# Kernel optimization log

Hardware: AMD Instinct MI355X
Metric: run time of the kernel (lower is better)

Reference implementation:

```python
import jax, jax.numpy as jnp
from jax import lax
import numpy as np

N, C, H, W = 8, 128, 96, 96
G, K = 8, 3                      # groups, kernel_size
GC = C // G                      # group channels = 16
STRIDE, PAD, DIL = 1, 1, 1
OFFSET_SCALE = 1.0
OM_DIM = int(np.ceil(G * K * K * 3 / 8) * 8)   # 216 (== G*K*K*3, no padding)
GN_EPS = 1e-5


def setup_inputs() -> dict:
    key = jax.random.key(0)
    ks = jax.random.split(key, 7)
    inp = {
        "input": jax.random.normal(ks[0], (N, C, H, W), dtype=jnp.float32),
        # depthwise conv (Conv2d groups=C): OIHW with I=1
        "dw_w": jax.random.normal(ks[1], (C, 1, K, K), dtype=jnp.float32) * 0.1,
        "dw_b": jax.random.normal(ks[2], (C,), dtype=jnp.float32) * 0.05,
        # GroupNorm(num_groups=1) affine params
        "gn_w": jnp.ones((C,), dtype=jnp.float32),
        "gn_b": jnp.zeros((C,), dtype=jnp.float32),
        # offset_mask Linear (module zero-inits; use small random for a meaningful test)
        "om_w": jax.random.normal(ks[3], (OM_DIM, C), dtype=jnp.float32) * 0.02,
        "om_b": jax.random.normal(ks[4], (OM_DIM,), dtype=jnp.float32) * 0.02,
    }
    return inp


def _dcnv4_forward(x, dw_w, dw_b, gn_w, gn_b, om_w, om_b):
    # x: (N, C, H, W)
    # ---- offset/mask branch: depthwise conv -> GroupNorm(1) -> GELU -> Linear
    x1 = lax.conv_general_dilated(
        x, dw_w, window_strides=(1, 1), padding=[(1, 1), (1, 1)],
        feature_group_count=C, dimension_numbers=("NCHW", "OIHW", "NCHW"))
    x1 = x1 + dw_b[None, :, None, None]
    mu = jnp.mean(x1, axis=(1, 2, 3), keepdims=True)
    var = jnp.var(x1, axis=(1, 2, 3), keepdims=True)
    x1 = (x1 - mu) * lax.rsqrt(var + GN_EPS)
    x1 = x1 * gn_w[None, :, None, None] + gn_b[None, :, None, None]
    x1 = jax.nn.gelu(x1, approximate=False)
    x1 = jnp.transpose(x1, (0, 2, 3, 1))                     # (N,H,W,C)
    om = jnp.einsum("nhwc,oc->nhwo", x1, om_w) + om_b        # (N,H,W,216)

    K2 = K * K
    om = om[..., : G * K2 * 3].reshape(N, H, W, G, K2 * 3)
    offs = om[..., : 2 * K2].reshape(N, H, W, G, K2, 2)      # (dx, dy) per point
    mask = om[..., 2 * K2:]                                  # (N,H,W,G,K2), no softmax in DCNv4

    # ---- sampling locations (pixel coords in the unpadded input, zeros outside)
    ky, kx = jnp.meshgrid(jnp.arange(K), jnp.arange(K), indexing="ij")
    base_y = ((ky - (K - 1) / 2.0) * DIL).reshape(-1).astype(jnp.float32)  # (K2,)
    base_x = ((kx - (K - 1) / 2.0) * DIL).reshape(-1).astype(jnp.float32)
    ctr_y = jnp.arange(H, dtype=jnp.float32) * STRIDE - PAD + DIL * (K - 1) / 2.0
    ctr_x = jnp.arange(W, dtype=jnp.float32) * STRIDE - PAD + DIL * (K - 1) / 2.0
    loc_y = ctr_y[None, :, None, None, None] + (base_y + offs[..., 1]) * OFFSET_SCALE
    loc_x = ctr_x[None, None, :, None, None] + (base_x + offs[..., 0]) * OFFSET_SCALE

    # ---- grouped bilinear gather
    xv = jnp.transpose(x, (0, 2, 3, 1)).reshape(N, H, W, G, GC)   # values, channels-last
    y0 = jnp.floor(loc_y)
    x0 = jnp.floor(loc_x)
    ly = loc_y - y0
    lx = loc_x - x0
    y0i = y0.astype(jnp.int32)
    x0i = x0.astype(jnp.int32)
    n_idx = jnp.arange(N)[:, None, None, None, None]
    g_idx = jnp.arange(G)[None, None, None, :, None]

    def gather(yi, xi):
        valid = (yi >= 0) & (yi < H) & (xi >= 0) & (xi < W)
        yc = jnp.clip(yi, 0, H - 1)
        xc = jnp.clip(xi, 0, W - 1)
        v = xv[n_idx, yc, xc, g_idx]                 # (N,H,W,G,K2,GC)
        return v * valid[..., None].astype(xv.dtype)

    samp = (gather(y0i,     x0i)     * ((1 - ly) * (1 - lx))[..., None]
          + gather(y0i,     x0i + 1) * ((1 - ly) * lx)[..., None]
          + gather(y0i + 1, x0i)     * (ly * (1 - lx))[..., None]
          + gather(y0i + 1, x0i + 1) * (ly * lx)[..., None])

    out = jnp.sum(samp * mask[..., None], axis=4)    # (N,H,W,G,GC)
    out = out.reshape(N, H, W, C)
    return jnp.transpose(out, (0, 3, 1, 2))          # (N,C,H,W)


def reference(input, dw_w, dw_b, gn_w, gn_b, om_w, om_b):
    return _dcnv4_forward(input, dw_w, dw_b, gn_w, gn_b, om_w, om_b)
```

## Files before the change

### kernel.cpp

```cpp
#include <hip/hip_runtime.h>

#define N_   8
#define C_   128
#define H_   96
#define W_   96
#define G_   8
#define GC_  16
#define HW_  (H_ * W_)
#define CHW_ (C_ * HW_)
#define OM_  216
#define OMP_ 224
#define OMROWS2_ 112
#define EPS_ 1e-5f
#define BLKS_PER_N_ 1152

typedef short bf16x8 __attribute__((ext_vector_type(8)));
typedef float f32x4 __attribute__((ext_vector_type(4)));

#if __has_builtin(__builtin_amdgcn_fdot2_f32_bf16)
#define HAVE_DOT2_ 1
typedef __bf16 bf16x2 __attribute__((ext_vector_type(2)));
static __device__ __forceinline__ bf16x2 u2bf2(unsigned int u) {
  union { unsigned int i; bf16x2 v; } c;
  c.i = u;
  return c.v;
}
#else
#define HAVE_DOT2_ 0
#endif

static __device__ __forceinline__ unsigned short f2bf(float f) {
  unsigned int u = __float_as_uint(f);
  unsigned int r = (u + 0x7fffu + ((u >> 16) & 1u)) >> 16;
  return (unsigned short)r;
}
static __device__ __forceinline__ float lo_bf(unsigned int u) {
  return __uint_as_float(u << 16);
}
static __device__ __forceinline__ float hi_bf(unsigned int u) {
  return __uint_as_float(u & 0xffff0000u);
}

__global__ __launch_bounds__(256) void k_front(const float* __restrict__ x,
                                               const float* __restrict__ dw_w,
                                               const float* __restrict__ dw_b,
                                               unsigned short* __restrict__ xgb,
                                               unsigned short* __restrict__ x1b,
                                               float2* __restrict__ partials) {
  __shared__ float tile_c[32][33];
  __shared__ float tile_a[32][33];
  __shared__ float ls[4], lq[4];
  int tx = threadIdx.x;
  int ty = threadIdx.y;
  int p0 = blockIdx.x * 32;
  int c0 = blockIdx.y * 32;
  int n = blockIdx.z;
  int p = p0 + tx;
  int h = p / W_;
  int w = p - h * W_;

  float s = 0.0f, q = 0.0f;
#pragma unroll
  for (int i = 0; i < 4; ++i) {
    int c = c0 + ty + i * 8;
    const float* wp = dw_w + c * 9;
    const float* xp = x + (n * C_ + c) * HW_;
    float acc = dw_b[c];
    float center = 0.0f;
#pragma unroll
    for (int dy = 0; dy < 3; ++dy) {
#pragma unroll
      for (int dx = 0; dx < 3; ++dx) {
        int yy = h + dy - 1;
        int xx = w + dx - 1;
        bool v = (yy >= 0) & (yy < H_) & (xx >= 0) & (xx < W_);
        float xin = v ? xp[yy * W_ + xx] : 0.0f;
        if (dy == 1 && dx == 1) center = xin;
        acc = fmaf(xin, wp[dy * 3 + dx], acc);
      }
    }
    tile_c[ty + i * 8][tx] = center;
    tile_a[ty + i * 8][tx] = acc;
    s += acc;
    q += acc * acc;
  }

  int tid = ty * 32 + tx;
#pragma unroll
  for (int o = 32; o > 0; o >>= 1) {
    s += __shfl_down(s, o);
    q += __shfl_down(q, o);
  }
  int lane = tid & 63;
  int wv = tid >> 6;
  if (lane == 0) { ls[wv] = s; lq[wv] = q; }
  __syncthreads();
  if (tid == 0) {
    int bid = blockIdx.x + 288 * blockIdx.y + BLKS_PER_N_ * n;
    partials[bid] = make_float2(ls[0] + ls[1] + ls[2] + ls[3],
                                lq[0] + lq[1] + lq[2] + lq[3]);
  }

  int c = c0 + tx;
  int g = c >> 4;
  int cc = c & 15;
#pragma unroll
  for (int i = 0; i < 4; ++i) {
    int pp = p0 + ty + i * 8;
    xgb[(((size_t)(n * G_ + g) * HW_) + pp) * GC_ + cc] = f2bf(tile_c[tx][ty + i * 8]);
    x1b[((size_t)(n * HW_) + pp) * C_ + c] = f2bf(tile_a[tx][ty + i * 8]);
  }
}

__global__ __launch_bounds__(256) void k_stats(const float2* __restrict__ partials,
                                               float* __restrict__ stats) {
  int n = blockIdx.x;
  int tid = threadIdx.x;
  const float2* p = partials + n * BLKS_PER_N_;
  float s = 0.0f, q = 0.0f;
  for (int i = tid; i < BLKS_PER_N_; i += 256) {
    float2 v = p[i];
    s += v.x;
    q += v.y;
  }
#pragma unroll
  for (int o = 32; o > 0; o >>= 1) {
    s += __shfl_down(s, o);
    q += __shfl_down(q, o);
  }
  __shared__ float ls[4], lq[4];
  int lane = tid & 63;
  int wv = tid >> 6;
  if (lane == 0) { ls[wv] = s; lq[wv] = q; }
  __syncthreads();
  if (tid == 0) {
    stats[n * 2 + 0] = ls[0] + ls[1] + ls[2] + ls[3];
    stats[n * 2 + 1] = lq[0] + lq[1] + lq[2] + lq[3];
  }
}

__global__ __launch_bounds__(256) void k_prep(const float* __restrict__ om_w,
                                              const float* __restrict__ om_b,
                                              unsigned short* __restrict__ A,
                                              float* __restrict__ biasp) {
  int idx = blockIdx.x * 256 + threadIdx.x;
  int o = idx >> 7;
  int cix = idx & 127;
  int g = o / 28;
  int k = o - g * 28;
  float v = (k < 27) ? om_w[(g * 27 + k) * C_ + cix] : 0.0f;
  A[idx] = f2bf(v);
  if (cix == 0) biasp[o] = (k < 27) ? om_b[g * 27 + k] : 0.0f;
}

__global__ __launch_bounds__(256) void k_gemm_mfma(const unsigned short* __restrict__ Bt,
                                                   const unsigned short* __restrict__ A,
                                                   const float* __restrict__ biasp,
                                                   const float* __restrict__ stats,
                                                   const float* __restrict__ gn_w,
                                                   const float* __restrict__ gn_b,
                                                   unsigned int* __restrict__ om2) {
  __shared__ unsigned short Bl[128 * 136];
  int tid = threadIdx.x;
  int pb = blockIdx.x;
  int n = blockIdx.y;
  int p0 = pb * 128;

  float sum = stats[n * 2 + 0];
  float ssq = stats[n * 2 + 1];
  const float inv = 1.0f / (float)CHW_;
  float mean = sum * inv;
  float var = ssq * inv - mean * mean;
  float rstd = rsqrtf(var + EPS_);
  int cbase = (tid & 15) * 8;
  float a8[8], b8[8];
#pragma unroll
  for (int j = 0; j < 8; ++j) {
    float gw = gn_w[cbase + j];
    float gb = gn_b[cbase + j];
    a8[j] = rstd * gw;
    b8[j] = gb - mean * rstd * gw;
  }

  const unsigned short* src = Bt + ((size_t)n * HW_ + p0) * C_;
#pragma unroll
  for (int i = 0; i < 8; ++i) {
    int idx = i * 256 + tid;
    int row = idx >> 4;
    int col = idx & 15;
    uint4 raw = *(const uint4*)(src + row * C_ + col * 8);
    unsigned int d[4] = {raw.x, raw.y, raw.z, raw.w};
    unsigned int od[4];
#pragma unroll
    for (int t = 0; t < 4; ++t) {
      float v0 = lo_bf(d[t]);
      float v1 = hi_bf(d[t]);
      float z0 = fmaf(v0, a8[2 * t], b8[2 * t]);
      float z1 = fmaf(v1, a8[2 * t + 1], b8[2 * t + 1]);
      float g0 = 0.5f * z0 * (1.0f + erff(z0 * 0.70710678118654752f));
      float g1 = 0.5f * z1 * (1.0f + erff(z1 * 0.70710678118654752f));
      od[t] = (unsigned int)f2bf(g0) | ((unsigned int)f2bf(g1) << 16);
    }
    uint4 packed = {od[0], od[1], od[2], od[3]};
    *(uint4*)(&Bl[row * 136 + col * 8]) = packed;
  }
  __syncthreads();

  int wave = tid >> 6;
  int lane = tid & 63;
  int quad = lane >> 4;
  int l16 = lane & 15;
  int pw = wave * 32;

  bf16x8 bfrag[2][4];
#pragma unroll
  for (int st = 0; st < 2; ++st) {
    int prow = pw + st * 16 + l16;
#pragma unroll
    for (int kk = 0; kk < 4; ++kk)
      bfrag[st][kk] = *(const bf16x8*)(&Bl[prow * 136 + kk * 32 + quad * 8]);
  }

  for (int ot = 0; ot < 14; ++ot) {
    const unsigned short* Ap = A + (ot * 16 + l16) * C_ + quad * 8;
    bf16x8 afrag[4];
#pragma unroll
    for (int kk = 0; kk < 4; ++kk)
      afrag[kk] = *(const bf16x8*)(Ap + kk * 32);

    f32x4 acc[2] = {{0.f, 0.f, 0.f, 0.f}, {0.f, 0.f, 0.f, 0.f}};
#pragma unroll
    for (int st = 0; st < 2; ++st)
#pragma unroll
      for (int kk = 0; kk < 4; ++kk)
        acc[st] = __builtin_amdgcn_mfma_f32_16x16x32_bf16(afrag[kk], bfrag[st][kk], acc[st], 0, 0, 0);

    int o0 = ot * 16 + quad * 4;
    float4 bv = *(const float4*)(biasp + o0);
#pragma unroll
    for (int st = 0; st < 2; ++st) {
      int p = p0 + pw + st * 16 + l16;
      unsigned int pk0 = (unsigned int)f2bf(acc[st][0] + bv.x) |
                         ((unsigned int)f2bf(acc[st][1] + bv.y) << 16);
      unsigned int pk1 = (unsigned int)f2bf(acc[st][2] + bv.z) |
                         ((unsigned int)f2bf(acc[st][3] + bv.w) << 16);
      unsigned int* Cp = om2 + ((size_t)n * OMROWS2_ + (o0 >> 1)) * HW_ + p;
      Cp[0] = pk0;
      Cp[HW_] = pk1;
    }
  }
}

__global__ __launch_bounds__(256) void k_sample(const unsigned short* __restrict__ xgb,
                                                const unsigned int* __restrict__ om2,
                                                float* __restrict__ out) {
  __shared__ int4 s_wa[9 * 64];

  int tid = threadIdx.x;
  int ord = blockIdx.x;
  int n = ord & 7;
  int t2 = ord >> 3;
  int g = t2 & 7;
  int pb = t2 >> 3;
  int p0 = pb * 64;

  const unsigned int* omb = om2 + ((size_t)n * OMROWS2_ + g * 14) * HW_ + p0;
  for (int j = tid; j < 576; j += 256) {
    int pt = j >> 6;
    int px = j & 63;
    int p = p0 + px;
    int h = p / W_;
    int w = p - h * W_;
    unsigned int od = omb[pt * HW_ + px];
    float offx = lo_bf(od);
    float offy = hi_bf(od);
    unsigned int md = omb[(9 + (pt >> 1)) * HW_ + px];
    float m = (pt & 1) ? hi_bf(md) : lo_bf(md);
    float locy = (float)(h + pt / 3 - 1) + offy;
    float locx = (float)(w + pt % 3 - 1) + offx;
    float y0f = floorf(locy);
    float x0f = floorf(locx);
    float ly = locy - y0f;
    float lx = locx - x0f;
    int y0 = (int)y0f;
    int x0 = (int)x0f;
    int y1 = y0 + 1;
    int x1 = x0 + 1;
    bool vy0 = (y0 >= 0) & (y0 < H_);
    bool vy1 = (y1 >= 0) & (y1 < H_);
    bool vx0 = (x0 >= 0) & (x0 < W_);
    bool vx1 = (x1 >= 0) & (x1 < W_);
    float t0 = (1.0f - ly) * m;
    float t1 = ly * m;
    float u0 = 1.0f - lx;
    float w00 = (vy0 & vx0) ? t0 * u0 : 0.0f;
    float w01 = (vy0 & vx1) ? t0 * lx : 0.0f;
    float w10 = (vy1 & vx0) ? t1 * u0 : 0.0f;
    float w11 = (vy1 & vx1) ? t1 * lx : 0.0f;
    int yc0 = min(max(y0, 0), H_ - 1);
    int yc1 = min(max(y1, 0), H_ - 1);
    int xs  = min(max(x0, 0), W_ - 2);
    int idx0 = min(max(x0, 0), W_ - 1) - xs;
    int idx1 = min(max(x1, 0), W_ - 1) - xs;
    float wr0y0 = (idx0 == 0 ? w00 : 0.0f) + (idx1 == 0 ? w01 : 0.0f);
    float wr1y0 = (idx0 == 1 ? w00 : 0.0f) + (idx1 == 1 ? w01 : 0.0f);
    float wr0y1 = (idx0 == 0 ? w10 : 0.0f) + (idx1 == 0 ? w11 : 0.0f);
    float wr1y1 = (idx0 == 1 ? w10 : 0.0f) + (idx1 == 1 ? w11 : 0.0f);
    int4 wa;
    wa.x = (int)((unsigned int)f2bf(wr0y0) | ((unsigned int)f2bf(wr0y1) << 16));
    wa.y = (int)((unsigned int)f2bf(wr1y0) | ((unsigned int)f2bf(wr1y1) << 16));
    wa.z = (yc0 * W_ + xs) * GC_;
    wa.w = (yc1 * W_ + xs) * GC_;
    s_wa[j] = wa;
  }
  __syncthreads();

  int px_l = tid >> 2;
  int sub = tid & 3;
  int rowhalf = sub >> 1;
  int chunk = sub & 1;
  int p = p0 + px_l;
  const unsigned short* xbb = xgb + ((size_t)(n * G_ + g) * HW_) * GC_;

  float acc[8] = {0, 0, 0, 0, 0, 0, 0, 0};
#pragma unroll
  for (int pt = 0; pt < 9; ++pt) {
    int4 wa = s_wa[pt * 64 + px_l];
    unsigned int aw = (unsigned int)(rowhalf ? wa.y : wa.x);
    uint4 r0 = *(const uint4*)(xbb + wa.z + sub * 8);
    uint4 r1 = *(const uint4*)(xbb + wa.w + sub * 8);
    unsigned int d0[4] = {r0.x, r0.y, r0.z, r0.w};
    unsigned int d1[4] = {r1.x, r1.y, r1.z, r1.w};
#if HAVE_DOT2_
    bf16x2 a2 = u2bf2(aw);
#pragma unroll
    for (int t = 0; t < 4; ++t) {
      unsigned int blo = __builtin_amdgcn_perm(d1[t], d0[t], 0x05040100u);
      unsigned int bhi = __builtin_amdgcn_perm(d1[t], d0[t], 0x07060302u);
      acc[2 * t]     = __builtin_amdgcn_fdot2_f32_bf16(a2, u2bf2(blo), acc[2 * t], false);
      acc[2 * t + 1] = __builtin_amdgcn_fdot2_f32_bf16(a2, u2bf2(bhi), acc[2 * t + 1], false);
    }
#else
    float w0 = lo_bf(aw);
    float w1 = hi_bf(aw);
#pragma unroll
    for (int t = 0; t < 4; ++t) {
      acc[2 * t]     = fmaf(w0, lo_bf(d0[t]), acc[2 * t]);
      acc[2 * t + 1] = fmaf(w0, hi_bf(d0[t]), acc[2 * t + 1]);
      acc[2 * t]     = fmaf(w1, lo_bf(d1[t]), acc[2 * t]);
      acc[2 * t + 1] = fmaf(w1, hi_bf(d1[t]), acc[2 * t + 1]);
    }
#endif
  }

#pragma unroll
  for (int i = 0; i < 8; ++i) acc[i] += __shfl_xor(acc[i], 2);

  int ch = chunk * 8 + rowhalf * 4;
  float* op = out + ((size_t)(n * C_ + g * GC_ + ch)) * HW_ + p;
#pragma unroll
  for (int r = 0; r < 4; ++r) op[r * HW_] = acc[rowhalf * 4 + r];
}

extern "C" void kernel_launch(void* const* d_in, const int* in_sizes, int n_in,
                              void* d_out, int out_size, void* d_ws, size_t ws_size,
                              hipStream_t stream) {
  const float* x    = (const float*)d_in[0];
  const float* dw_w = (const float*)d_in[1];
  const float* dw_b = (const float*)d_in[2];
  const float* gn_w = (const float*)d_in[3];
  const float* gn_b = (const float*)d_in[4];
  const float* om_w = (const float*)d_in[5];
  const float* om_b = (const float*)d_in[6];
  float* out = (float*)d_out;

  unsigned short* xgb = (unsigned short*)d_ws;
  unsigned short* x1b = xgb + (size_t)N_ * CHW_;
  unsigned int* om2 = (unsigned int*)(x1b + (size_t)N_ * CHW_);
  float* stats = (float*)(om2 + (size_t)N_ * OMROWS2_ * HW_);
  float2* partials = (float2*)(stats + 16);
  unsigned short* Abf = (unsigned short*)(partials + N_ * BLKS_PER_N_);
  float* biasp = (float*)(Abf + OMP_ * C_);

  k_front<<<dim3(HW_ / 32, C_ / 32, N_), dim3(32, 8), 0, stream>>>(
      x, dw_w, dw_b, xgb, x1b, partials);
  k_stats<<<N_, 256, 0, stream>>>(partials, stats);
  k_prep<<<(OMP_ * C_) / 256, 256, 0, stream>>>(om_w, om_b, Abf, biasp);
  k_gemm_mfma<<<dim3(HW_ / 128, N_), 256, 0, stream>>>(
      x1b, Abf, biasp, stats, gn_w, gn_b, om2);
  k_sample<<<9216, 256, 0, stream>>>(xgb, om2, out);
}
```

Before: 197.2 us.

## Shrink GEMM pixel tile, split output tiles across waves, use fast GELU

The GEMM kernel's pixel tile drops from 128 to 32 pixels per block, giving four times as many blocks. The four waves now split the work as 2 pixel halves by 2 output-tile halves instead of each wave owning 32 pixels across all 14 output tiles. Bias is staged in shared memory, and the exact erff in GELU is replaced by a rational erf approximation built on a hardware reciprocal and a fast exp. The goal is better occupancy and latency hiding plus cheaper transcendental work. The cost is reloading the A fragments in more blocks and a small loss of accuracy in GELU before bf16 rounding.

```diff
diff --git a/kernel.cpp b/kernel.cpp
--- a/kernel.cpp
+++ b/kernel.cpp
@@ -39,6 +39,19 @@
 }
 static __device__ __forceinline__ float hi_bf(unsigned int u) {
   return __uint_as_float(u & 0xffff0000u);
+}
+
+static __device__ __forceinline__ float fast_gelu(float z) {
+  float s = z * 0.70710678118654752f;
+  float as = fabsf(s);
+  float t = __builtin_amdgcn_rcpf(fmaf(0.3275911f, as, 1.0f));
+  float e = __expf(-as * as);
+  float inner = fmaf(fmaf(fmaf(fmaf(1.061405429f, t, -1.453152027f), t,
+                               1.421413741f), t, -0.284496736f), t, 0.254829592f);
+  float y = fmaf(-inner * t, e, 1.0f);
+  float erf_s = copysignf(y, s);
+  float hz = 0.5f * z;
+  return fmaf(hz, erf_s, hz);
 }
 
 __global__ __launch_bounds__(256) void k_front(const float* __restrict__ x,
@@ -160,11 +173,16 @@
                                                    const float* __restrict__ gn_w,
                                                    const float* __restrict__ gn_b,
                                                    unsigned int* __restrict__ om2) {
-  __shared__ unsigned short Bl[128 * 136];
+  __shared__ unsigned short Bl[32 * 136];
+  __shared__ alignas(16) float s_bias[OMP_];
   int tid = threadIdx.x;
   int pb = blockIdx.x;
   int n = blockIdx.y;
-  int p0 = pb * 128;
+  int p0 = pb * 32;
+
+  if (tid < OMP_ / 4) {
+    ((float4*)s_bias)[tid] = ((const float4*)biasp)[tid];
+  }
 
   float sum = stats[n * 2 + 0];
   float ssq = stats[n * 2 + 1];
@@ -184,7 +202,7 @@
 
   const unsigned short* src = Bt + ((size_t)n * HW_ + p0) * C_;
 #pragma unroll
-  for (int i = 0; i < 8; ++i) {
+  for (int i = 0; i < 2; ++i) {
     int idx = i * 256 + tid;
     int row = idx >> 4;
     int col = idx & 15;
@@ -197,8 +215,8 @@
       float v1 = hi_bf(d[t]);
       float z0 = fmaf(v0, a8[2 * t], b8[2 * t]);
       float z1 = fmaf(v1, a8[2 * t + 1], b8[2 * t + 1]);
-      float g0 = 0.5f * z0 * (1.0f + erff(z0 * 0.70710678118654752f));
-      float g1 = 0.5f * z1 * (1.0f + erff(z1 * 0.70710678118654752f));
+      float g0 = fast_gelu(z0);
+      float g1 = fast_gelu(z1);
       od[t] = (unsigned int)f2bf(g0) | ((unsigned int)f2bf(g1) << 16);
     }
     uint4 packed = {od[0], od[1], od[2], od[3]};
@@ -210,44 +228,38 @@
   int lane = tid & 63;
   int quad = lane >> 4;
   int l16 = lane & 15;
-  int pw = wave * 32;
-
-  bf16x8 bfrag[2][4];
-#pragma unroll
-  for (int st = 0; st < 2; ++st) {
-    int prow = pw + st * 16 + l16;
-#pragma unroll
-    for (int kk = 0; kk < 4; ++kk)
-      bfrag[st][kk] = *(const bf16x8*)(&Bl[prow * 136 + kk * 32 + quad * 8]);
-  }
-
-  for (int ot = 0; ot < 14; ++ot) {
+  int pixhalf = wave & 1;
+  int othalf = wave >> 1;
+  int prow = pixhalf * 16 + l16;
+
+  bf16x8 bfrag[4];
+#pragma unroll
+  for (int kk = 0; kk < 4; ++kk)
+    bfrag[kk] = *(const bf16x8*)(&Bl[prow * 136 + kk * 32 + quad * 8]);
+
+  int p = p0 + prow;
+  for (int oi = 0; oi < 7; ++oi) {
+    int ot = othalf * 7 + oi;
     const unsigned short* Ap = A + (ot * 16 + l16) * C_ + quad * 8;
     bf16x8 afrag[4];
 #pragma unroll
     for (int kk = 0; kk < 4; ++kk)
       afrag[kk] = *(const bf16x8*)(Ap + kk * 32);
 
-    f32x4 acc[2] = {{0.f, 0.f, 0.f, 0.f}, {0.f, 0.f, 0.f, 0.f}};
-#pragma unroll
-    for (int st = 0; st < 2; ++st)
-#pragma unroll
-      for (int kk = 0; kk < 4; ++kk)
-        acc[st] = __builtin_amdgcn_mfma_f32_16x16x32_bf16(afrag[kk], bfrag[st][kk], acc[st], 0, 0, 0);
+    f32x4 acc = {0.f, 0.f, 0.f, 0.f};
+#pragma unroll
+    for (int kk = 0; kk < 4; ++kk)
+      acc = __builtin_amdgcn_mfma_f32_16x16x32_bf16(afrag[kk], bfrag[kk], acc, 0, 0, 0);
 
     int o0 = ot * 16 + quad * 4;
-    float4 bv = *(const float4*)(biasp + o0);
-#pragma unroll
-    for (int st = 0; st < 2; ++st) {
-      int p = p0 + pw + st * 16 + l16;
-      unsigned int pk0 = (unsigned int)f2bf(acc[st][0] + bv.x) |
-                         ((unsigned int)f2bf(acc[st][1] + bv.y) << 16);
-      unsigned int pk1 = (unsigned int)f2bf(acc[st][2] + bv.z) |
-                         ((unsigned int)f2bf(acc[st][3] + bv.w) << 16);
-      unsigned int* Cp = om2 + ((size_t)n * OMROWS2_ + (o0 >> 1)) * HW_ + p;
-      Cp[0] = pk0;
-      Cp[HW_] = pk1;
-    }
+    float4 bv = *(const float4*)(&s_bias[o0]);
+    unsigned int pk0 = (unsigned int)f2bf(acc[0] + bv.x) |
+                       ((unsigned int)f2bf(acc[1] + bv.y) << 16);
+    unsigned int pk1 = (unsigned int)f2bf(acc[2] + bv.z) |
+                       ((unsigned int)f2bf(acc[3] + bv.w) << 16);
+    unsigned int* Cp = om2 + ((size_t)n * OMROWS2_ + (o0 >> 1)) * HW_ + p;
+    Cp[0] = pk0;
+    Cp[HW_] = pk1;
   }
 }
 
@@ -386,7 +398,7 @@
       x, dw_w, dw_b, xgb, x1b, partials);
   k_stats<<<N_, 256, 0, stream>>>(partials, stats);
   k_prep<<<(OMP_ * C_) / 256, 256, 0, stream>>>(om_w, om_b, Abf, biasp);
-  k_gemm_mfma<<<dim3(HW_ / 128, N_), 256, 0, stream>>>(
+  k_gemm_mfma<<<dim3(HW_ / 32, N_), 256, 0, stream>>>(
       x1b, Abf, biasp, stats, gn_w, gn_b, om2);
   k_sample<<<9216, 256, 0, stream>>>(xgb, om2, out);
 }
```

New measurement: 197.7 us. Within noise of the previous version (+0.3%).
